# Kernel optimization log

Hardware: AMD Instinct MI355X
Metric: run time of the kernel (lower is better)

Reference implementation:

```python
import jax, jax.numpy as jnp
import numpy as np

N, L, H, K, T = 768, 8, 64, 4, 3

def _mlp2(x, w1, b1, w2, b2):
    # Linear -> ReLU -> Linear -> ReLU (matches nn.Sequential in q/k/v MLPs)
    return jax.nn.relu(jax.nn.relu(x @ w1 + b1) @ w2 + b2)

def setup_inputs() -> dict:
    key = jax.random.key(0)
    ks = jax.random.split(key, 20)
    s = 1.0 / np.sqrt(H)
    def lin(k, din, dout):
        return jax.random.uniform(k, (din, dout), jnp.float32, -s, s)
    def bias(k, dout):
        return jax.random.uniform(k, (dout,), jnp.float32, -s, s)
    inp = {
        "h": jax.random.normal(ks[0], (N, L, H), jnp.float32),
        "coord": jax.random.normal(ks[1], (N, L, K, T), jnp.float32),
        "wq1": lin(ks[2], H, H), "bq1": bias(ks[3], H),
        "wq2": lin(ks[4], H, H), "bq2": bias(ks[5], H),
        "wk1": lin(ks[6], H, H), "bk1": bias(ks[7], H),
        "wk2": lin(ks[8], H, H), "bk2": bias(ks[9], H),
        "wv1": lin(ks[10], H, H), "bv1": bias(ks[11], H),
        "wv2": lin(ks[12], H, H), "bv2": bias(ks[13], H),
        "wc1": lin(ks[14], H, H), "bc1": bias(ks[15], H),
        # final coord layer: Linear(H, 4, bias=False), xavier gain=0.001
        "wc2": jax.random.normal(ks[16], (H, K), jnp.float32) * 0.001,
    }
    return inp

def reference(h, coord, wq1, bq1, wq2, bq2, wk1, bk1, wk2, bk2,
              wv1, bv1, wv2, bv2, wc1, bc1, wc2):
    q = _mlp2(h, wq1, bq1, wq2, bq2)          # [N, L, H]
    k = _mlp2(h, wk1, bk1, wk2, bk2)          # [N, L, H]
    v = _mlp2(h, wv1, bv1, wv2, bv2)          # [N, L, H]
    # scores[i, j, l] = <q_i, k_j> per frame l; softmax over neighbor axis j (dim=1)
    scores = jnp.einsum('ilh,jlh->ijl', q, k)
    alpha = jax.nn.softmax(scores, axis=1)     # [N, N, L]
    h_agg = jnp.einsum('ijl,jlh->ilh', alpha, v)
    cmv = jax.nn.relu(v @ wc1 + bc1) @ wc2     # coord_mlp(v): [N, L, 4]
    coord_diff = coord[:, None] - coord[None]  # [N, N, L, 4, 3]
    x_agg = jnp.einsum('ijlkt,ijl,jlk->ilkt', coord_diff, alpha, cmv)
    return (h + h_agg, coord + x_agg)
```

## Files before the change

kernel.cpp:

```cpp
#include <hip/hip_runtime.h>
#include <hip/hip_bf16.h>

#define NN 768
#define LL 8
#define HH 64
#define IT 16
#define ABP 776
#define XST 80

typedef __attribute__((ext_vector_type(8))) short bf16x8;
typedef __attribute__((ext_vector_type(4))) float f32x4;

__device__ __forceinline__ short f2bf(float x) {
    union { __hip_bfloat16 h; short s; } u;
    u.h = __float2bfloat16(x);
    return u.s;
}

__device__ __forceinline__ bf16x8 pack8(float4 lo, float4 hi) {
    bf16x8 r;
    r[0] = f2bf(lo.x); r[1] = f2bf(lo.y); r[2] = f2bf(lo.z); r[3] = f2bf(lo.w);
    r[4] = f2bf(hi.x); r[5] = f2bf(hi.y); r[6] = f2bf(hi.z); r[7] = f2bf(hi.w);
    return r;
}

__device__ __forceinline__ void layer_mfma(bf16x8 a0, bf16x8 a1,
                                           const float* __restrict__ W,
                                           const float* __restrict__ bias,
                                           int m, int quad, bool do_relu,
                                           f32x4 dout[4])
{
    #pragma unroll
    for (int nt = 0; nt < 4; ++nt) {
        const int n = nt * 16 + m;
        const float* wp = W + (quad * 8) * 64 + n;
        bf16x8 b0, b1;
        #pragma unroll
        for (int j = 0; j < 8; ++j) b0[j] = f2bf(wp[j * 64]);
        #pragma unroll
        for (int j = 0; j < 8; ++j) b1[j] = f2bf(wp[(32 + j) * 64]);
        f32x4 d = {0.f, 0.f, 0.f, 0.f};
        d = __builtin_amdgcn_mfma_f32_16x16x32_bf16(a0, b0, d, 0, 0, 0);
        d = __builtin_amdgcn_mfma_f32_16x16x32_bf16(a1, b1, d, 0, 0, 0);
        if (bias) {
            const float bb = bias[n];
            #pragma unroll
            for (int rg = 0; rg < 4; ++rg) d[rg] += bb;
        }
        if (do_relu) {
            #pragma unroll
            for (int rg = 0; rg < 4; ++rg) d[rg] = fmaxf(d[rg], 0.f);
        }
        dout[nt] = d;
    }
}

__device__ __forceinline__ void d_to_X(const f32x4 d[4], short (*X)[XST],
                                       int m, int quad) {
    #pragma unroll
    for (int nt = 0; nt < 4; ++nt)
        #pragma unroll
        for (int rg = 0; rg < 4; ++rg)
            X[quad * 4 + rg][nt * 16 + m] = f2bf(d[nt][rg]);
}

__global__ __launch_bounds__(256) void qkv_kernel(
    const float* __restrict__ h, const float* __restrict__ coord,
    const float* __restrict__ wq1, const float* __restrict__ bq1,
    const float* __restrict__ wq2, const float* __restrict__ bq2,
    const float* __restrict__ wk1, const float* __restrict__ bk1,
    const float* __restrict__ wk2, const float* __restrict__ bk2,
    const float* __restrict__ wv1, const float* __restrict__ bv1,
    const float* __restrict__ wv2, const float* __restrict__ bv2,
    const float* __restrict__ wc1, const float* __restrict__ bc1,
    const float* __restrict__ wc2,
    short* __restrict__ q_ws, short* __restrict__ k_ws,
    short* __restrict__ vT_ws, short* __restrict__ UT_ws)
{
    const int lane = threadIdx.x & 63;
    const int w    = threadIdx.x >> 6;
    const int wid  = blockIdx.x * 4 + w;
    const int chain = wid / 384;
    const int rt    = wid - chain * 384;
    const int r0    = rt * 16;

    const int m    = lane & 15;
    const int quad = lane >> 4;

    __shared__ short Xs[4][16][XST];
    __shared__ float cms[4][16][4];
    short (*X)[XST] = Xs[w];

    bf16x8 a0, a1;
    {
        const float* hrow = h + (size_t)(r0 + m) * 64;
        a0 = pack8(*(const float4*)(hrow + quad * 8),
                   *(const float4*)(hrow + quad * 8 + 4));
        a1 = pack8(*(const float4*)(hrow + 32 + quad * 8),
                   *(const float4*)(hrow + 32 + quad * 8 + 4));
    }

    f32x4 d[4];

    if (chain == 0) {
        layer_mfma(a0, a1, wq1, bq1, m, quad, true, d);
        d_to_X(d, X, m, quad);
        __builtin_amdgcn_wave_barrier();
        a0 = *(const bf16x8*)&X[m][quad * 8];
        a1 = *(const bf16x8*)&X[m][32 + quad * 8];
        layer_mfma(a0, a1, wq2, bq2, m, quad, true, d);
        #pragma unroll
        for (int nt = 0; nt < 4; ++nt)
            #pragma unroll
            for (int rg = 0; rg < 4; ++rg) {
                const int g = r0 + quad * 4 + rg, i = g >> 3, l = g & 7;
                q_ws[(l * NN + i) * 64 + nt * 16 + m] = f2bf(d[nt][rg]);
            }
    } else if (chain == 1) {
        layer_mfma(a0, a1, wk1, bk1, m, quad, true, d);
        d_to_X(d, X, m, quad);
        __builtin_amdgcn_wave_barrier();
        a0 = *(const bf16x8*)&X[m][quad * 8];
        a1 = *(const bf16x8*)&X[m][32 + quad * 8];
        layer_mfma(a0, a1, wk2, bk2, m, quad, true, d);
        #pragma unroll
        for (int nt = 0; nt < 4; ++nt)
            #pragma unroll
            for (int rg = 0; rg < 4; ++rg) {
                const int g = r0 + quad * 4 + rg, i = g >> 3, l = g & 7;
                k_ws[(l * NN + i) * 64 + nt * 16 + m] = f2bf(d[nt][rg]);
            }
    } else {
        layer_mfma(a0, a1, wv1, bv1, m, quad, true, d);
        d_to_X(d, X, m, quad);
        __builtin_amdgcn_wave_barrier();
        a0 = *(const bf16x8*)&X[m][quad * 8];
        a1 = *(const bf16x8*)&X[m][32 + quad * 8];
        layer_mfma(a0, a1, wv2, bv2, m, quad, true, d);
        #pragma unroll
        for (int nt = 0; nt < 4; ++nt)
            #pragma unroll
            for (int rg = 0; rg < 4; ++rg) {
                const int g = r0 + quad * 4 + rg, i = g >> 3, l = g & 7;
                vT_ws[((size_t)l * 64 + nt * 16 + m) * NN + i] = f2bf(d[nt][rg]);
            }
        d_to_X(d, X, m, quad);
        __builtin_amdgcn_wave_barrier();
        a0 = *(const bf16x8*)&X[m][quad * 8];
        a1 = *(const bf16x8*)&X[m][32 + quad * 8];
        layer_mfma(a0, a1, wc1, bc1, m, quad, true, d);
        d_to_X(d, X, m, quad);
        __builtin_amdgcn_wave_barrier();
        a0 = *(const bf16x8*)&X[m][quad * 8];
        a1 = *(const bf16x8*)&X[m][32 + quad * 8];
        {
            bf16x8 b0, b1;
            #pragma unroll
            for (int j = 0; j < 8; ++j) {
                b0[j] = (m < 4) ? f2bf(wc2[(quad * 8 + j) * 4 + m]) : (short)0;
                b1[j] = (m < 4) ? f2bf(wc2[(32 + quad * 8 + j) * 4 + m]) : (short)0;
            }
            f32x4 dc = {0.f, 0.f, 0.f, 0.f};
            dc = __builtin_amdgcn_mfma_f32_16x16x32_bf16(a0, b0, dc, 0, 0, 0);
            dc = __builtin_amdgcn_mfma_f32_16x16x32_bf16(a1, b1, dc, 0, 0, 0);
            if (m < 4) {
                #pragma unroll
                for (int rg = 0; rg < 4; ++rg)
                    cms[w][quad * 4 + rg][m] = dc[rg];
            }
        }
        __builtin_amdgcn_wave_barrier();
        {
            const int row = lane >> 2, kk = lane & 3;
            const float c = cms[w][row][kk];
            const int g = r0 + row, i = g >> 3, l = g & 7;
            UT_ws[((size_t)l * 16 + kk * 4 + 0) * NN + i] = f2bf(c);
            #pragma unroll
            for (int seg = 1; seg < 4; ++seg) {
                const float uval = c * coord[g * 12 + kk * 3 + (seg - 1)];
                UT_ws[((size_t)l * 16 + kk * 4 + seg) * NN + i] = f2bf(uval);
            }
        }
    }
}

__global__ __launch_bounds__(256) void attn_kernel(
    const short* __restrict__ q_ws, const short* __restrict__ k_ws,
    const short* __restrict__ vT_ws, const short* __restrict__ UT_ws,
    const float* __restrict__ h, const float* __restrict__ coord,
    float* __restrict__ h_out, float* __restrict__ x_out)
{
    const int l    = blockIdx.x & 7;
    const int i0   = (blockIdx.x >> 3) * IT;
    const int t    = threadIdx.x;
    const int lane = t & 63;
    const int w    = t >> 6;
    const int m    = lane & 15;
    const int quad = lane >> 4;

    __shared__ alignas(16) short al[IT][ABP];
    __shared__ float wmax[4][IT];
    __shared__ float wsum[4][IT];
    __shared__ float part3[4][IT][16];
    __shared__ float smS[IT][16];

    const bf16x8 aq0 = *(const bf16x8*)&q_ws[((size_t)l * NN + i0 + m) * 64 + quad * 8];
    const bf16x8 aq1 = *(const bf16x8*)&q_ws[((size_t)l * NN + i0 + m) * 64 + 32 + quad * 8];

    f32x4 dsc[12];
    {
        const short* kl = k_ws + (size_t)l * NN * 64;
        #pragma unroll
        for (int nt = 0; nt < 12; ++nt) {
            const int jb = 192 * w + nt * 16;
            const short* krow = kl + (size_t)(jb + m) * 64;
            bf16x8 b0 = *(const bf16x8*)(krow + quad * 8);
            bf16x8 b1 = *(const bf16x8*)(krow + 32 + quad * 8);
            f32x4 d = {0.f, 0.f, 0.f, 0.f};
            d = __builtin_amdgcn_mfma_f32_16x16x32_bf16(aq0, b0, d, 0, 0, 0);
            d = __builtin_amdgcn_mfma_f32_16x16x32_bf16(aq1, b1, d, 0, 0, 0);
            dsc[nt] = d;
        }
    }

    float mx[4];
    #pragma unroll
    for (int rg = 0; rg < 4; ++rg) {
        float mm = dsc[0][rg];
        #pragma unroll
        for (int nt = 1; nt < 12; ++nt) mm = fmaxf(mm, dsc[nt][rg]);
        mm = fmaxf(mm, __shfl_xor(mm, 1, 64));
        mm = fmaxf(mm, __shfl_xor(mm, 2, 64));
        mm = fmaxf(mm, __shfl_xor(mm, 4, 64));
        mm = fmaxf(mm, __shfl_xor(mm, 8, 64));
        if (m == 0) wmax[w][quad * 4 + rg] = mm;
    }
    __syncthreads();
    #pragma unroll
    for (int rg = 0; rg < 4; ++rg) {
        const int row = quad * 4 + rg;
        mx[rg] = fmaxf(fmaxf(wmax[0][row], wmax[1][row]),
                       fmaxf(wmax[2][row], wmax[3][row]));
    }

    float sl[4] = {0.f, 0.f, 0.f, 0.f};
    #pragma unroll
    for (int nt = 0; nt < 12; ++nt) {
        const int jb = 192 * w + nt * 16;
        #pragma unroll
        for (int rg = 0; rg < 4; ++rg) {
            const float e = __expf(dsc[nt][rg] - mx[rg]);
            sl[rg] += e;
            al[quad * 4 + rg][jb + m] = f2bf(e);
        }
    }
    #pragma unroll
    for (int rg = 0; rg < 4; ++rg) {
        float s = sl[rg];
        s += __shfl_xor(s, 1, 64);
        s += __shfl_xor(s, 2, 64);
        s += __shfl_xor(s, 4, 64);
        s += __shfl_xor(s, 8, 64);
        if (m == 0) wsum[w][quad * 4 + rg] = s;
    }
    __syncthreads();

    {
        f32x4 acc0 = {0.f, 0.f, 0.f, 0.f};
        f32x4 acc1 = {0.f, 0.f, 0.f, 0.f};
        const short* vrow = vT_ws + ((size_t)l * 64 + 16 * w + m) * NN;
        #pragma unroll 4
        for (int kt = 0; kt < 24; kt += 2) {
            const int ka = kt * 32, kb = ka + 32;
            bf16x8 a0 = *(const bf16x8*)&al[m][ka + quad * 8];
            bf16x8 b0 = *(const bf16x8*)(vrow + ka + quad * 8);
            bf16x8 a1 = *(const bf16x8*)&al[m][kb + quad * 8];
            bf16x8 b1 = *(const bf16x8*)(vrow + kb + quad * 8);
            acc0 = __builtin_amdgcn_mfma_f32_16x16x32_bf16(a0, b0, acc0, 0, 0, 0);
            acc1 = __builtin_amdgcn_mfma_f32_16x16x32_bf16(a1, b1, acc1, 0, 0, 0);
        }
        const int c = 16 * w + m;
        #pragma unroll
        for (int rg = 0; rg < 4; ++rg) {
            const int i = quad * 4 + rg;
            const float ri = 1.f / (wsum[0][i] + wsum[1][i] +
                                    wsum[2][i] + wsum[3][i]);
            const int row = ((i0 + i) * 8 + l) * 64 + c;
            h_out[row] = h[row] + ri * (acc0[rg] + acc1[rg]);
        }
    }

    {
        f32x4 acc = {0.f, 0.f, 0.f, 0.f};
        const short* urow = UT_ws + ((size_t)l * 16 + m) * NN + 192 * w;
        #pragma unroll
        for (int kt = 0; kt < 6; ++kt) {
            const int k0 = kt * 32;
            bf16x8 a = *(const bf16x8*)&al[m][192 * w + k0 + quad * 8];
            bf16x8 b = *(const bf16x8*)(urow + k0 + quad * 8);
            acc = __builtin_amdgcn_mfma_f32_16x16x32_bf16(a, b, acc, 0, 0, 0);
        }
        #pragma unroll
        for (int rg = 0; rg < 4; ++rg)
            part3[w][quad * 4 + rg][m] = acc[rg];
    }
    __syncthreads();
    {
        const int i = t >> 4, u = t & 15;
        const float ri = 1.f / (wsum[0][i] + wsum[1][i] +
                                wsum[2][i] + wsum[3][i]);
        smS[i][u] = (part3[0][i][u] + part3[1][i][u] +
                     part3[2][i][u] + part3[3][i][u]) * ri;
    }
    __syncthreads();
    if (t < 192) {
        const int i4 = t / 12, kt = t % 12, k4 = kt / 3, s4 = kt % 3;
        const int idx = ((i0 + i4) * 8 + l) * 12 + kt;
        const float cd = coord[idx];
        x_out[idx] = cd + cd * smS[i4][k4 * 4] - smS[i4][k4 * 4 + 1 + s4];
    }
}

extern "C" void kernel_launch(void* const* d_in, const int* in_sizes, int n_in,
                              void* d_out, int out_size, void* d_ws, size_t ws_size,
                              hipStream_t stream) {
    const float* h     = (const float*)d_in[0];
    const float* coord = (const float*)d_in[1];

    float* h_out = (float*)d_out;
    float* x_out = h_out + NN * LL * HH;

    short* q_ws  = (short*)d_ws;
    short* k_ws  = q_ws + NN * LL * HH;
    short* vT_ws = k_ws + NN * LL * HH;
    short* UT_ws = vT_ws + NN * LL * HH;

    qkv_kernel<<<288, 256, 0, stream>>>(
        h, coord,
        (const float*)d_in[2],  (const float*)d_in[3],
        (const float*)d_in[4],  (const float*)d_in[5],
        (const float*)d_in[6],  (const float*)d_in[7],
        (const float*)d_in[8],  (const float*)d_in[9],
        (const float*)d_in[10], (const float*)d_in[11],
        (const float*)d_in[12], (const float*)d_in[13],
        (const float*)d_in[14], (const float*)d_in[15],
        (const float*)d_in[16],
        q_ws, k_ws, vT_ws, UT_ws);

    attn_kernel<<<(NN / IT) * LL, 256, 0, stream>>>(
        q_ws, k_ws, vT_ws, UT_ws, h, coord, h_out, x_out);
}
```

Baseline: 114.0 us.

## Stage MLP weights in LDS, prefetch V/U/h/coord operands, drop reduction barrier

In the QKV kernel each block now converts its chain's weight matrices to bf16 once in shared memory, instead of every wave doing strided global loads per tile. Blocks are regrouped so each block holds a single chain, with the V chain blocks scheduled first, and coord values are prefetched early. The attention kernel issues its V^T and U operand loads plus its h and coord loads before the softmax, so their latency overlaps the exp work. It also folds the final partial-sum reduction into the output step, removing one __syncthreads and the smS buffer, and adds a launch bound of 2 blocks per SM. The price is higher register pressure from the 30 prefetched bf16x8 values and extra LDS for the staged weights.

```diff
diff --git a/kernel.cpp b/kernel.cpp
--- a/kernel.cpp
+++ b/kernel.cpp
@@ -7,6 +7,7 @@
 #define IT 16
 #define ABP 776
 #define XST 80
+#define WST 72
 
 typedef __attribute__((ext_vector_type(8))) short bf16x8;
 typedef __attribute__((ext_vector_type(4))) float f32x4;
@@ -24,21 +25,26 @@
     return r;
 }
 
-__device__ __forceinline__ void layer_mfma(bf16x8 a0, bf16x8 a1,
-                                           const float* __restrict__ W,
-                                           const float* __restrict__ bias,
-                                           int m, int quad, bool do_relu,
-                                           f32x4 dout[4])
+__device__ __forceinline__ void stage_W(short (*Wt)[WST],
+                                        const float* __restrict__ W, int t) {
+    const int n  = t & 63;
+    const int kb = (t >> 6) * 16;
+    #pragma unroll
+    for (int jj = 0; jj < 16; ++jj)
+        Wt[n][kb + jj] = f2bf(W[(kb + jj) * 64 + n]);
+}
+
+__device__ __forceinline__ void layer_mfma_lds(bf16x8 a0, bf16x8 a1,
+                                               const short (*Wt)[WST],
+                                               const float* __restrict__ bias,
+                                               int m, int quad, bool do_relu,
+                                               f32x4 dout[4])
 {
     #pragma unroll
     for (int nt = 0; nt < 4; ++nt) {
         const int n = nt * 16 + m;
-        const float* wp = W + (quad * 8) * 64 + n;
-        bf16x8 b0, b1;
-        #pragma unroll
-        for (int j = 0; j < 8; ++j) b0[j] = f2bf(wp[j * 64]);
-        #pragma unroll
-        for (int j = 0; j < 8; ++j) b1[j] = f2bf(wp[(32 + j) * 64]);
+        bf16x8 b0 = *(const bf16x8*)&Wt[n][quad * 8];
+        bf16x8 b1 = *(const bf16x8*)&Wt[n][32 + quad * 8];
         f32x4 d = {0.f, 0.f, 0.f, 0.f};
         d = __builtin_amdgcn_mfma_f32_16x16x32_bf16(a0, b0, d, 0, 0, 0);
         d = __builtin_amdgcn_mfma_f32_16x16x32_bf16(a1, b1, d, 0, 0, 0);
@@ -77,17 +83,23 @@
     short* __restrict__ q_ws, short* __restrict__ k_ws,
     short* __restrict__ vT_ws, short* __restrict__ UT_ws)
 {
-    const int lane = threadIdx.x & 63;
-    const int w    = threadIdx.x >> 6;
-    const int wid  = blockIdx.x * 4 + w;
-    const int chain = wid / 384;
-    const int rt    = wid - chain * 384;
-    const int r0    = rt * 16;
+    const int t    = threadIdx.x;
+    const int lane = t & 63;
+    const int w    = t >> 6;
+
+    const int bb = blockIdx.x;
+    int chain, tb;
+    if (bb < 96)       { chain = 2; tb = bb; }
+    else if (bb < 192) { chain = 0; tb = bb - 96; }
+    else               { chain = 1; tb = bb - 192; }
+    const int rt = tb * 4 + w;
+    const int r0 = rt * 16;
 
     const int m    = lane & 15;
     const int quad = lane >> 4;
 
-    __shared__ short Xs[4][16][XST];
+    __shared__ alignas(16) short Wt[3][64][WST];
+    __shared__ alignas(16) short Xs[4][16][XST];
     __shared__ float cms[4][16][4];
     short (*X)[XST] = Xs[w];
 
@@ -100,15 +112,30 @@
                    *(const float4*)(hrow + 32 + quad * 8 + 4));
     }
 
+    float cpre[3];
+    const int rowu = lane >> 2, kk = lane & 3;
+    const int gu = r0 + rowu;
+    if (chain == 2) {
+        #pragma unroll
+        for (int s = 0; s < 3; ++s)
+            cpre[s] = coord[gu * 12 + kk * 3 + s];
+    }
+
+    if (chain == 0)      { stage_W(Wt[0], wq1, t); stage_W(Wt[1], wq2, t); }
+    else if (chain == 1) { stage_W(Wt[0], wk1, t); stage_W(Wt[1], wk2, t); }
+    else                 { stage_W(Wt[0], wv1, t); stage_W(Wt[1], wv2, t);
+                           stage_W(Wt[2], wc1, t); }
+    __syncthreads();
+
     f32x4 d[4];
 
     if (chain == 0) {
-        layer_mfma(a0, a1, wq1, bq1, m, quad, true, d);
-        d_to_X(d, X, m, quad);
-        __builtin_amdgcn_wave_barrier();
-        a0 = *(const bf16x8*)&X[m][quad * 8];
-        a1 = *(const bf16x8*)&X[m][32 + quad * 8];
-        layer_mfma(a0, a1, wq2, bq2, m, quad, true, d);
+        layer_mfma_lds(a0, a1, Wt[0], bq1, m, quad, true, d);
+        d_to_X(d, X, m, quad);
+        __builtin_amdgcn_wave_barrier();
+        a0 = *(const bf16x8*)&X[m][quad * 8];
+        a1 = *(const bf16x8*)&X[m][32 + quad * 8];
+        layer_mfma_lds(a0, a1, Wt[1], bq2, m, quad, true, d);
         #pragma unroll
         for (int nt = 0; nt < 4; ++nt)
             #pragma unroll
@@ -117,12 +144,12 @@
                 q_ws[(l * NN + i) * 64 + nt * 16 + m] = f2bf(d[nt][rg]);
             }
     } else if (chain == 1) {
-        layer_mfma(a0, a1, wk1, bk1, m, quad, true, d);
-        d_to_X(d, X, m, quad);
-        __builtin_amdgcn_wave_barrier();
-        a0 = *(const bf16x8*)&X[m][quad * 8];
-        a1 = *(const bf16x8*)&X[m][32 + quad * 8];
-        layer_mfma(a0, a1, wk2, bk2, m, quad, true, d);
+        layer_mfma_lds(a0, a1, Wt[0], bk1, m, quad, true, d);
+        d_to_X(d, X, m, quad);
+        __builtin_amdgcn_wave_barrier();
+        a0 = *(const bf16x8*)&X[m][quad * 8];
+        a1 = *(const bf16x8*)&X[m][32 + quad * 8];
+        layer_mfma_lds(a0, a1, Wt[1], bk2, m, quad, true, d);
         #pragma unroll
         for (int nt = 0; nt < 4; ++nt)
             #pragma unroll
@@ -131,12 +158,12 @@
                 k_ws[(l * NN + i) * 64 + nt * 16 + m] = f2bf(d[nt][rg]);
             }
     } else {
-        layer_mfma(a0, a1, wv1, bv1, m, quad, true, d);
-        d_to_X(d, X, m, quad);
-        __builtin_amdgcn_wave_barrier();
-        a0 = *(const bf16x8*)&X[m][quad * 8];
-        a1 = *(const bf16x8*)&X[m][32 + quad * 8];
-        layer_mfma(a0, a1, wv2, bv2, m, quad, true, d);
+        layer_mfma_lds(a0, a1, Wt[0], bv1, m, quad, true, d);
+        d_to_X(d, X, m, quad);
+        __builtin_amdgcn_wave_barrier();
+        a0 = *(const bf16x8*)&X[m][quad * 8];
+        a1 = *(const bf16x8*)&X[m][32 + quad * 8];
+        layer_mfma_lds(a0, a1, Wt[1], bv2, m, quad, true, d);
         #pragma unroll
         for (int nt = 0; nt < 4; ++nt)
             #pragma unroll
@@ -148,7 +175,7 @@
         __builtin_amdgcn_wave_barrier();
         a0 = *(const bf16x8*)&X[m][quad * 8];
         a1 = *(const bf16x8*)&X[m][32 + quad * 8];
-        layer_mfma(a0, a1, wc1, bc1, m, quad, true, d);
+        layer_mfma_lds(a0, a1, Wt[2], bc1, m, quad, true, d);
         d_to_X(d, X, m, quad);
         __builtin_amdgcn_wave_barrier();
         a0 = *(const bf16x8*)&X[m][quad * 8];
@@ -171,20 +198,19 @@
         }
         __builtin_amdgcn_wave_barrier();
         {
-            const int row = lane >> 2, kk = lane & 3;
-            const float c = cms[w][row][kk];
-            const int g = r0 + row, i = g >> 3, l = g & 7;
+            const float c = cms[w][rowu][kk];
+            const int i = gu >> 3, l = gu & 7;
             UT_ws[((size_t)l * 16 + kk * 4 + 0) * NN + i] = f2bf(c);
             #pragma unroll
             for (int seg = 1; seg < 4; ++seg) {
-                const float uval = c * coord[g * 12 + kk * 3 + (seg - 1)];
+                const float uval = c * cpre[seg - 1];
                 UT_ws[((size_t)l * 16 + kk * 4 + seg) * NN + i] = f2bf(uval);
             }
         }
     }
 }
 
-__global__ __launch_bounds__(256) void attn_kernel(
+__global__ __launch_bounds__(256, 2) void attn_kernel(
     const short* __restrict__ q_ws, const short* __restrict__ k_ws,
     const short* __restrict__ vT_ws, const short* __restrict__ UT_ws,
     const float* __restrict__ h, const float* __restrict__ coord,
@@ -202,7 +228,15 @@
     __shared__ float wmax[4][IT];
     __shared__ float wsum[4][IT];
     __shared__ float part3[4][IT][16];
-    __shared__ float smS[IT][16];
+
+    const int c = 16 * w + m;
+    float hpre[4];
+    #pragma unroll
+    for (int rg = 0; rg < 4; ++rg)
+        hpre[rg] = h[((i0 + quad * 4 + rg) * 8 + l) * 64 + c];
+    float cdpre = 0.f;
+    if (t < 192)
+        cdpre = coord[((i0 + t / 12) * 8 + l) * 12 + (t % 12)];
 
     const bf16x8 aq0 = *(const bf16x8*)&q_ws[((size_t)l * NN + i0 + m) * 64 + quad * 8];
     const bf16x8 aq1 = *(const bf16x8*)&q_ws[((size_t)l * NN + i0 + m) * 64 + 32 + quad * 8];
@@ -243,6 +277,17 @@
                        fmaxf(wmax[2][row], wmax[3][row]));
     }
 
+    const short* vrow = vT_ws + ((size_t)l * 64 + 16 * w + m) * NN;
+    const short* urow = UT_ws + ((size_t)l * 16 + m) * NN + 192 * w;
+    bf16x8 vpre[24];
+    bf16x8 upre[6];
+    #pragma unroll
+    for (int kt = 0; kt < 24; ++kt)
+        vpre[kt] = *(const bf16x8*)(vrow + kt * 32 + quad * 8);
+    #pragma unroll
+    for (int kt = 0; kt < 6; ++kt)
+        upre[kt] = *(const bf16x8*)(urow + kt * 32 + quad * 8);
+
     float sl[4] = {0.f, 0.f, 0.f, 0.f};
     #pragma unroll
     for (int nt = 0; nt < 12; ++nt) {
@@ -268,56 +313,48 @@
     {
         f32x4 acc0 = {0.f, 0.f, 0.f, 0.f};
         f32x4 acc1 = {0.f, 0.f, 0.f, 0.f};
-        const short* vrow = vT_ws + ((size_t)l * 64 + 16 * w + m) * NN;
-        #pragma unroll 4
+        #pragma unroll
         for (int kt = 0; kt < 24; kt += 2) {
             const int ka = kt * 32, kb = ka + 32;
             bf16x8 a0 = *(const bf16x8*)&al[m][ka + quad * 8];
-            bf16x8 b0 = *(const bf16x8*)(vrow + ka + quad * 8);
             bf16x8 a1 = *(const bf16x8*)&al[m][kb + quad * 8];
-            bf16x8 b1 = *(const bf16x8*)(vrow + kb + quad * 8);
-            acc0 = __builtin_amdgcn_mfma_f32_16x16x32_bf16(a0, b0, acc0, 0, 0, 0);
-            acc1 = __builtin_amdgcn_mfma_f32_16x16x32_bf16(a1, b1, acc1, 0, 0, 0);
-        }
-        const int c = 16 * w + m;
+            acc0 = __builtin_amdgcn_mfma_f32_16x16x32_bf16(a0, vpre[kt], acc0, 0, 0, 0);
+            acc1 = __builtin_amdgcn_mfma_f32_16x16x32_bf16(a1, vpre[kt + 1], acc1, 0, 0, 0);
+        }
         #pragma unroll
         for (int rg = 0; rg < 4; ++rg) {
             const int i = quad * 4 + rg;
             const float ri = 1.f / (wsum[0][i] + wsum[1][i] +
                                     wsum[2][i] + wsum[3][i]);
             const int row = ((i0 + i) * 8 + l) * 64 + c;
-            h_out[row] = h[row] + ri * (acc0[rg] + acc1[rg]);
+            h_out[row] = hpre[rg] + ri * (acc0[rg] + acc1[rg]);
         }
     }
 
     {
         f32x4 acc = {0.f, 0.f, 0.f, 0.f};
-        const short* urow = UT_ws + ((size_t)l * 16 + m) * NN + 192 * w;
         #pragma unroll
         for (int kt = 0; kt < 6; ++kt) {
             const int k0 = kt * 32;
             bf16x8 a = *(const bf16x8*)&al[m][192 * w + k0 + quad * 8];
-            bf16x8 b = *(const bf16x8*)(urow + k0 + quad * 8);
-            acc = __builtin_amdgcn_mfma_f32_16x16x32_bf16(a, b, acc, 0, 0, 0);
+            acc = __builtin_amdgcn_mfma_f32_16x16x32_bf16(a, upre[kt], acc, 0, 0, 0);
         }
         #pragma unroll
         for (int rg = 0; rg < 4; ++rg)
             part3[w][quad * 4 + rg][m] = acc[rg];
-    }
-    __syncthreads();
-    {
-        const int i = t >> 4, u = t & 15;
-        const float ri = 1.f / (wsum[0][i] + wsum[1][i] +
-                                wsum[2][i] + wsum[3][i]);
-        smS[i][u] = (part3[0][i][u] + part3[1][i][u] +
-                     part3[2][i][u] + part3[3][i][u]) * ri;
     }
     __syncthreads();
     if (t < 192) {
         const int i4 = t / 12, kt = t % 12, k4 = kt / 3, s4 = kt % 3;
+        const float ri = 1.f / (wsum[0][i4] + wsum[1][i4] +
+                                wsum[2][i4] + wsum[3][i4]);
+        const int uA = k4 * 4, uB = k4 * 4 + 1 + s4;
+        const float sA = (part3[0][i4][uA] + part3[1][i4][uA] +
+                          part3[2][i4][uA] + part3[3][i4][uA]) * ri;
+        const float sB = (part3[0][i4][uB] + part3[1][i4][uB] +
+                          part3[2][i4][uB] + part3[3][i4][uB]) * ri;
         const int idx = ((i0 + i4) * 8 + l) * 12 + kt;
-        const float cd = coord[idx];
-        x_out[idx] = cd + cd * smS[i4][k4 * 4] - smS[i4][k4 * 4 + 1 + s4];
+        x_out[idx] = cdpre + cdpre * sA - sB;
     }
 }
 
```

Result: faster. 110.2 us (-3.3%).
